# Kernel optimization log

Measured on AMD Instinct MI355X. Metric: run time of the kernel, lower is better.

The kernel has to match this reference:

```python
import jax, jax.numpy as jnp
import numpy as np

N, T, D, K = 32, 8192, 64, 64
LOG2PI = float(np.log(2.0 * np.pi))


def setup_inputs() -> dict:
    key = jax.random.key(0)
    k1, k2, k3, k4 = jax.random.split(key, 4)
    x = jax.random.normal(k1, (N, T, D), dtype=jnp.float32)
    # valid GMM params: positive weights summing to 1, positive diagonal covariances
    weights = jax.nn.softmax(jax.random.normal(k2, (K,), dtype=jnp.float32))
    means = jax.random.normal(k3, (K, D), dtype=jnp.float32)
    covars = jax.random.uniform(k4, (K, D), dtype=jnp.float32, minval=0.5, maxval=1.5)
    return {"x": x, "weights": weights, "means": means, "covars": covars}


def _posterior(x, weights, means, covars):
    # diagonal-GMM predict_proba without materializing [N,T,K,D]:
    # sum_d (x-mu)^2/c = sum x^2/c - 2 sum x*mu/c + sum mu^2/c
    inv_c = 1.0 / covars                                   # [K,D]
    quad = (jnp.einsum('ntd,kd->ntk', x * x, inv_c)
            - 2.0 * jnp.einsum('ntd,kd->ntk', x, means * inv_c)
            + jnp.sum(means * means * inv_c, axis=-1))      # [N,T,K]
    log_prob = (jnp.log(weights)
                - 0.5 * (D * LOG2PI + jnp.sum(jnp.log(covars), axis=-1) + quad))
    return jax.nn.softmax(log_prob, axis=-1)               # [N,T,K]


def reference(x, weights, means, covars):
    # p = predict_proba * weights, renormalized over K (as in the torch code)
    p = _posterior(x, weights, means, covars) * weights
    p = p / jnp.sum(p, axis=-1, keepdims=True)             # [N,T,K]

    # pooled statistics over T (einsum avoids the [N,T,K,D] intermediate)
    s0 = jnp.sum(p, axis=1)                                # [N,K]
    s1 = jnp.einsum('ntk,ntd->nkd', p, x)                  # [N,K,D]
    s2 = jnp.einsum('ntk,ntd->nkd', p, x * x)              # [N,K,D]

    sw = jnp.sqrt(weights)                                 # [K]
    v0 = (s0 - T * weights) / sw                           # [N,K]
    v1 = (s1 - means * s0[..., None]) / (sw[:, None] * jnp.sqrt(covars))
    v2 = (s2 - 2.0 * means * s1 + (means ** 2 - covars) * s0[..., None]) / (
        jnp.sqrt(jnp.float32(2.0)) * sw[:, None] * covars)

    v = jnp.concatenate([v0[..., None], v1, v2], axis=2).reshape(x.shape[0], -1)
    # power normalization then L2 normalization
    v = jnp.sign(v) * jnp.sqrt(jnp.abs(v))
    v = v / jnp.linalg.norm(v, axis=1, keepdims=True)
    return v
```

## Files before the change

kernel.cpp:

```cpp
#include <hip/hip_runtime.h>
#include <math.h>

#define N_  32
#define T_  8192
#define D_  64
#define K_  64
#define CHUNKS 24
#define TB 64
#define STATS_PER_N (K_ + 2 * K_ * D_)
#define XSTR 72

typedef _Float16 half_t;
typedef __attribute__((ext_vector_type(8)))  _Float16 v8h;
typedef __attribute__((ext_vector_type(4)))  float    v4f;
typedef __attribute__((ext_vector_type(16))) float    v16f;

__global__ void prep_kernel(const float* __restrict__ w, const float* __restrict__ mu,
                            const float* __restrict__ cv, float* __restrict__ Ap,
                            half_t* __restrict__ WH, float* __restrict__ ssq) {
    if (blockIdx.x < 8) {
#pragma unroll
        for (int i = 0; i < 4; ++i) {
            const int e = blockIdx.x * 1024 + i * 256 + threadIdx.x;
            const int j = e & 7, l = (e >> 3) & 63, fs = e >> 9;
            const int tile = fs >> 2, s = fs & 3;
            const int kc = 16 * tile + (l & 15);
            const int f  = 32 * s + 8 * (l >> 4) + j;
            float val;
            if (f < 64) val = mu[kc * 64 + f] / cv[kc * 64 + f];
            else        val = -0.5f / cv[kc * 64 + (f - 64)];
            WH[e] = (half_t)val;
        }
    } else {
        if (threadIdx.x < 32) ssq[threadIdx.x] = 0.f;
        if (threadIdx.x < K_) {
            const int k = threadIdx.x;
            float acc = 0.f;
            for (int d = 0; d < D_; ++d) {
                const int idx = k * D_ + d;
                const float c = cv[idx], m = mu[idx];
                acc += logf(c) + m * m / c;
            }
            Ap[k] = 2.f * logf(w[k]) - 0.5f * acc;
        }
    }
}

__launch_bounds__(256, 3)
__global__ void main_kernel(const float* __restrict__ x, const float* __restrict__ Ap,
                            const half_t* __restrict__ WH, float* __restrict__ outbuf,
                            int mode) {
    __shared__ half_t Xs[2][TB][XSTR];
    __shared__ half_t Pt[2][K_][XSTR];
    __shared__ float  s0sh[4][64];

    const int tid  = threadIdx.x;
    const int lane = tid & 63;
    const int wv   = tid >> 6;
    const int chunk = blockIdx.x;
    const int n     = blockIdx.y;
    const int q     = lane >> 4;
    const int c0    = lane & 15;
    const int tok   = 16 * wv + c0;

    const int r3   = (3 - (n % 3)) % 3;
    const int hcnt = (chunk + 2 - r3) / 3;
    const int boff = 5 * chunk + hcnt;
    const int cnt  = 5 + ((chunk % 3) == r3 ? 1 : 0);

    v8h Wf[16];
#pragma unroll
    for (int t = 0; t < 4; ++t)
#pragma unroll
        for (int s = 0; s < 4; ++s)
            Wf[t * 4 + s] = *(const v8h*)(WH + (size_t)((t * 4 + s) * 64 + lane) * 8);

    float apv[16];
#pragma unroll
    for (int t = 0; t < 4; ++t)
#pragma unroll
        for (int r = 0; r < 4; ++r) apv[t * 4 + r] = Ap[16 * t + 4 * q + r];

    float S0loc[16];
#pragma unroll
    for (int j = 0; j < 16; ++j) S0loc[j] = 0.f;

    const int sig = wv >> 1;
    const int dh  = wv & 1;
    v16f accB[2];
#pragma unroll
    for (int m = 0; m < 2; ++m)
#pragma unroll
        for (int r = 0; r < 16; ++r) accB[m][r] = 0.f;

    const size_t xbase = ((size_t)n * T_ + (size_t)boff * TB) * (size_t)D_;
    const float* xrow0 = x + xbase + tok * 64 + 8 * q;

    float4 R[4];
    R[0] = *(const float4*)(xrow0);
    R[1] = *(const float4*)(xrow0 + 4);
    R[2] = *(const float4*)(xrow0 + 32);
    R[3] = *(const float4*)(xrow0 + 36);

#pragma unroll 1
    for (int batch = 0; batch < cnt; ++batch) {
        const int buf = batch & 1;
        v8h xh0, xh1, qh0, qh1;
        {
            const float4 a = R[0], b = R[1], c = R[2], d = R[3];
            xh0[0] = (half_t)a.x; xh0[1] = (half_t)a.y; xh0[2] = (half_t)a.z; xh0[3] = (half_t)a.w;
            xh0[4] = (half_t)b.x; xh0[5] = (half_t)b.y; xh0[6] = (half_t)b.z; xh0[7] = (half_t)b.w;
            xh1[0] = (half_t)c.x; xh1[1] = (half_t)c.y; xh1[2] = (half_t)c.z; xh1[3] = (half_t)c.w;
            xh1[4] = (half_t)d.x; xh1[5] = (half_t)d.y; xh1[6] = (half_t)d.z; xh1[7] = (half_t)d.w;
            qh0[0] = (half_t)(a.x * a.x); qh0[1] = (half_t)(a.y * a.y);
            qh0[2] = (half_t)(a.z * a.z); qh0[3] = (half_t)(a.w * a.w);
            qh0[4] = (half_t)(b.x * b.x); qh0[5] = (half_t)(b.y * b.y);
            qh0[6] = (half_t)(b.z * b.z); qh0[7] = (half_t)(b.w * b.w);
            qh1[0] = (half_t)(c.x * c.x); qh1[1] = (half_t)(c.y * c.y);
            qh1[2] = (half_t)(c.z * c.z); qh1[3] = (half_t)(c.w * c.w);
            qh1[4] = (half_t)(d.x * d.x); qh1[5] = (half_t)(d.y * d.y);
            qh1[6] = (half_t)(d.z * d.z); qh1[7] = (half_t)(d.w * d.w);
            *(v8h*)&Xs[buf][tok][8 * q]      = xh0;
            *(v8h*)&Xs[buf][tok][32 + 8 * q] = xh1;
        }

        if (batch + 1 < cnt) {
            const float* xr = xrow0 + (size_t)(batch + 1) * TB * D_;
            R[0] = *(const float4*)(xr);
            R[1] = *(const float4*)(xr + 4);
            R[2] = *(const float4*)(xr + 32);
            R[3] = *(const float4*)(xr + 36);
        }

        {
            v4f acc[4];
#pragma unroll
            for (int t = 0; t < 4; ++t) acc[t] = (v4f)(0.f);
#pragma unroll
            for (int t = 0; t < 4; ++t) {
                acc[t] = __builtin_amdgcn_mfma_f32_16x16x32_f16(Wf[t * 4 + 0], xh0, acc[t], 0, 0, 0);
                acc[t] = __builtin_amdgcn_mfma_f32_16x16x32_f16(Wf[t * 4 + 1], xh1, acc[t], 0, 0, 0);
                acc[t] = __builtin_amdgcn_mfma_f32_16x16x32_f16(Wf[t * 4 + 2], qh0, acc[t], 0, 0, 0);
                acc[t] = __builtin_amdgcn_mfma_f32_16x16x32_f16(Wf[t * 4 + 3], qh1, acc[t], 0, 0, 0);
            }
            float pv[16];
            float m = -1e30f;
#pragma unroll
            for (int t = 0; t < 4; ++t)
#pragma unroll
                for (int r = 0; r < 4; ++r) {
                    const float lg = acc[t][r] + apv[t * 4 + r];
                    pv[t * 4 + r] = lg;
                    m = fmaxf(m, lg);
                }
            m = fmaxf(m, __shfl_xor(m, 16, 64));
            m = fmaxf(m, __shfl_xor(m, 32, 64));
            float ssum = 0.f;
#pragma unroll
            for (int j = 0; j < 16; ++j) { pv[j] = __expf(pv[j] - m); ssum += pv[j]; }
            ssum += __shfl_xor(ssum, 16, 64);
            ssum += __shfl_xor(ssum, 32, 64);
            const float rs = 1.f / ssum;
#pragma unroll
            for (int j = 0; j < 16; ++j) { pv[j] *= rs; S0loc[j] += pv[j]; }
#pragma unroll
            for (int t = 0; t < 4; ++t)
#pragma unroll
                for (int r = 0; r < 4; ++r)
                    Pt[buf][16 * t + 4 * q + r][tok] = (half_t)pv[t * 4 + r];
        }
        __syncthreads();

        {
            const int m   = lane & 31;
            const int h   = lane >> 5;
            const int d   = 32 * dh + m;
            const half_t* Arow0 = &Pt[buf][m][0];
            const half_t* Arow1 = &Pt[buf][32 + m][0];
            const half_t* Bsrc  = &Xs[buf][0][0];
#pragma unroll
            for (int st = 0; st < 4; ++st) {
                const int tB = 16 * st + 8 * h;
                const v8h a0 = *(const v8h*)(Arow0 + tB);
                const v8h a1 = *(const v8h*)(Arow1 + tB);
                v8h bf;
#pragma unroll
                for (int j = 0; j < 8; ++j)
                    bf[j] = Bsrc[(tB + j) * XSTR + d];
                if (sig) bf = bf * bf;
                accB[0] = __builtin_amdgcn_mfma_f32_32x32x16_f16(a0, bf, accB[0], 0, 0, 0);
                accB[1] = __builtin_amdgcn_mfma_f32_32x32x16_f16(a1, bf, accB[1], 0, 0, 0);
            }
        }
    }

    __syncthreads();
#pragma unroll
    for (int j = 0; j < 16; ++j) {
        float v = S0loc[j];
        v += __shfl_xor(v, 1, 64);
        v += __shfl_xor(v, 2, 64);
        v += __shfl_xor(v, 4, 64);
        v += __shfl_xor(v, 8, 64);
        S0loc[j] = v;
    }
    if (c0 == 0) {
#pragma unroll
        for (int t = 0; t < 4; ++t)
#pragma unroll
            for (int r = 0; r < 4; ++r)
                s0sh[wv][16 * t + 4 * q + r] = S0loc[t * 4 + r];
    }
    __syncthreads();

    if (mode == 1) {
        float* dstb = outbuf + (size_t)(n * CHUNKS + chunk) * STATS_PER_N;
        if (tid < 64)
            dstb[tid] = s0sh[0][tid] + s0sh[1][tid] + s0sh[2][tid] + s0sh[3][tid];
        const int d = 32 * dh + (lane & 31);
        float* dst = dstb + 64 + sig * 4096;
#pragma unroll
        for (int mt = 0; mt < 2; ++mt)
#pragma unroll
            for (int r = 0; r < 16; ++r) {
                const int kc = 32 * mt + (r & 3) + 8 * (r >> 2) + 4 * (lane >> 5);
                dst[kc * 64 + d] = accB[mt][r];
            }
    } else {
        float* sb = outbuf + (size_t)n * STATS_PER_N;
        if (tid < 64)
            atomicAdd(&sb[tid], s0sh[0][tid] + s0sh[1][tid] + s0sh[2][tid] + s0sh[3][tid]);
        const int d = 32 * dh + (lane & 31);
        float* dst = sb + 64 + sig * 4096;
#pragma unroll
        for (int mt = 0; mt < 2; ++mt)
#pragma unroll
            for (int r = 0; r < 16; ++r) {
                const int kc = 32 * mt + (r & 3) + 8 * (r >> 2) + 4 * (lane >> 5);
                atomicAdd(&dst[kc * 64 + d], accB[mt][r]);
            }
    }
}

__global__ void reduce_pow_kernel(const float* __restrict__ partials,
                                  const float* __restrict__ w, const float* __restrict__ mu,
                                  const float* __restrict__ cv,
                                  float* __restrict__ us, float* __restrict__ ssq) {
    __shared__ float red[4];
    const int e = blockIdx.x * 256 + threadIdx.x;
    const int n = blockIdx.y;
    float u = 0.f;
    if (e < STATS_PER_N) {
        const float* base = partials + (size_t)n * CHUNKS * STATS_PER_N;
        float sv = 0.f;
#pragma unroll 8
        for (int c = 0; c < CHUNKS; ++c) sv += base[(size_t)c * STATS_PER_N + e];
        float v; int oidx;
        if (e < 64) {
            const float wv = w[e];
            v = (sv - (float)T_ * wv) * rsqrtf(wv);
            oidx = e * 129;
        } else if (e < 64 + 4096) {
            const int idx = e - 64, k = idx >> 6, d = idx & 63;
            float s0v = 0.f;
#pragma unroll 8
            for (int c = 0; c < CHUNKS; ++c) s0v += base[(size_t)c * STATS_PER_N + k];
            v = (sv - mu[idx] * s0v) * rsqrtf(w[k] * cv[idx]);
            oidx = k * 129 + 1 + d;
        } else {
            const int idx = e - 4160, k = idx >> 6, d = idx & 63;
            float s0v = 0.f, s1v = 0.f;
#pragma unroll 4
            for (int c = 0; c < CHUNKS; ++c) {
                s0v += base[(size_t)c * STATS_PER_N + k];
                s1v += base[(size_t)c * STATS_PER_N + 64 + idx];
            }
            const float m_ = mu[idx], c_ = cv[idx];
            v = (sv - 2.f * m_ * s1v + (m_ * m_ - c_) * s0v) * (rsqrtf(2.f * w[k]) / c_);
            oidx = k * 129 + 65 + d;
        }
        u = (v >= 0.f) ? sqrtf(v) : -sqrtf(-v);
        us[(size_t)n * STATS_PER_N + oidx] = u;
    }
    float ss = u * u;
#pragma unroll
    for (int off = 32; off > 0; off >>= 1) ss += __shfl_xor(ss, off, 64);
    if ((threadIdx.x & 63) == 0) red[threadIdx.x >> 6] = ss;
    __syncthreads();
    if (threadIdx.x == 0)
        atomicAdd(&ssq[n], red[0] + red[1] + red[2] + red[3]);
}

__global__ void scale_kernel(const float* __restrict__ us, const float* __restrict__ ssq,
                             float* __restrict__ out) {
    const int e = blockIdx.x * 256 + threadIdx.x;
    const int n = blockIdx.y;
    if (e < STATS_PER_N)
        out[(size_t)n * STATS_PER_N + e] = us[(size_t)n * STATS_PER_N + e] * rsqrtf(ssq[n]);
}

__global__ void fin_kernel(const float* __restrict__ w, const float* __restrict__ mu,
                           const float* __restrict__ cv, const float* __restrict__ stats,
                           float* __restrict__ out) {
    __shared__ float us[STATS_PER_N];
    __shared__ float red[4];
    const int n   = blockIdx.x;
    const int tid = threadIdx.x;
    const float* sb = stats + (size_t)n * STATS_PER_N;

    float ss = 0.f;
    if (tid < 64) {
        const float wv = w[tid];
        const float v = (sb[tid] - (float)T_ * wv) * rsqrtf(wv);
        const float u = (v >= 0.f) ? sqrtf(v) : -sqrtf(-v);
        us[tid * 129] = u;
        ss = fmaf(u, u, ss);
    }
#pragma unroll 1
    for (int i = 0; i < 16; ++i) {
        const int idx = i * 256 + tid;
        const int k = idx >> 6, d = idx & 63;
        const float v = (sb[64 + idx] - mu[idx] * sb[k]) * rsqrtf(w[k] * cv[idx]);
        const float u = (v >= 0.f) ? sqrtf(v) : -sqrtf(-v);
        us[k * 129 + 1 + d] = u;
        ss = fmaf(u, u, ss);
    }
#pragma unroll 1
    for (int i = 0; i < 16; ++i) {
        const int idx = i * 256 + tid;
        const int k = idx >> 6, d = idx & 63;
        const float m_ = mu[idx], c_ = cv[idx];
        const float s1v = sb[64 + idx], s2v = sb[64 + 4096 + idx];
        const float v = (s2v - 2.f * m_ * s1v + (m_ * m_ - c_) * sb[k]) *
                        (rsqrtf(2.f * w[k]) / c_);
        const float u = (v >= 0.f) ? sqrtf(v) : -sqrtf(-v);
        us[k * 129 + 65 + d] = u;
        ss = fmaf(u, u, ss);
    }
#pragma unroll
    for (int off = 32; off > 0; off >>= 1) ss += __shfl_xor(ss, off, 64);
    if ((tid & 63) == 0) red[tid >> 6] = ss;
    __syncthreads();
    const float tot = red[0] + red[1] + red[2] + red[3];
    const float rn = rsqrtf(tot);
    for (int e = tid; e < STATS_PER_N; e += 256)
        out[(size_t)n * STATS_PER_N + e] = us[e] * rn;
}

extern "C" void kernel_launch(void* const* d_in, const int* in_sizes, int n_in,
                              void* d_out, int out_size, void* d_ws, size_t ws_size,
                              hipStream_t stream) {
    const float* x  = (const float*)d_in[0];
    const float* w  = (const float*)d_in[1];
    const float* mu = (const float*)d_in[2];
    const float* cv = (const float*)d_in[3];
    float* out = (float*)d_out;

    const size_t part_elems = (size_t)CHUNKS * N_ * STATS_PER_N;
    const size_t us_elems   = (size_t)N_ * STATS_PER_N;
    const size_t need_big = (part_elems + us_elems + 32 + K_ + (size_t)K_ * 64) * sizeof(float);

    if (ws_size >= need_big) {
        float* partials = (float*)d_ws;
        float* us  = partials + part_elems;
        float* ssq = us + us_elems;
        float* Ap  = ssq + 32;
        half_t* WH = (half_t*)(Ap + K_);

        prep_kernel<<<9, 256, 0, stream>>>(w, mu, cv, Ap, WH, ssq);
        main_kernel<<<dim3(CHUNKS, N_), 256, 0, stream>>>(x, Ap, WH, partials, 1);
        reduce_pow_kernel<<<dim3(33, N_), 256, 0, stream>>>(partials, w, mu, cv, us, ssq);
        scale_kernel<<<dim3(33, N_), 256, 0, stream>>>(us, ssq, out);
    } else {
        float* stats = (float*)d_ws;
        float* ssq = stats + us_elems;
        float* Ap  = ssq + 32;
        half_t* WH = (half_t*)(Ap + K_);

        hipMemsetAsync(stats, 0, us_elems * sizeof(float), stream);
        prep_kernel<<<9, 256, 0, stream>>>(w, mu, cv, Ap, WH, ssq);
        main_kernel<<<dim3(CHUNKS, N_), 256, 0, stream>>>(x, Ap, WH, stats, 0);
        fin_kernel<<<N_, 256, 0, stream>>>(w, mu, cv, stats, out);
    }
}
```

Measured before the change: 150.5 us.

## Split main kernel into producer and consumer waves with skewed pipeline

Waves 0-1 now act as producers. Each handles two 16-token groups: it converts x to fp16, runs the logit MFMAs and the softmax, and writes P and X to LDS. Waves 2-3 act as consumers and accumulate the s1 and s2 MFMAs for the previous batch. This lets both stages overlap with one barrier per step. It also folds the Ap bias into the accumulator init, squares x in half precision, and uses a lighter LDS-only barrier. The intended gain is overlapping the two phases, at the cost of less parallelism per stage, higher register pressure in consumers (four 32x32 accumulators), and an fp16 squaring precision change.

```diff
diff --git a/kernel.cpp b/kernel.cpp
--- a/kernel.cpp
+++ b/kernel.cpp
@@ -14,6 +14,11 @@
 typedef __attribute__((ext_vector_type(8)))  _Float16 v8h;
 typedef __attribute__((ext_vector_type(4)))  float    v4f;
 typedef __attribute__((ext_vector_type(16))) float    v16f;
+
+#define BAR_LDS() do {                                                  \
+    asm volatile("s_waitcnt lgkmcnt(0)" ::: "memory");                  \
+    __builtin_amdgcn_s_barrier();                                       \
+} while (0)
 
 __global__ void prep_kernel(const float* __restrict__ w, const float* __restrict__ mu,
                             const float* __restrict__ cv, float* __restrict__ Ap,
@@ -52,193 +57,204 @@
                             int mode) {
     __shared__ half_t Xs[2][TB][XSTR];
     __shared__ half_t Pt[2][K_][XSTR];
-    __shared__ float  s0sh[4][64];
+    __shared__ float  s0sh[2][64];
 
     const int tid  = threadIdx.x;
     const int lane = tid & 63;
     const int wv   = tid >> 6;
     const int chunk = blockIdx.x;
     const int n     = blockIdx.y;
-    const int q     = lane >> 4;
-    const int c0    = lane & 15;
-    const int tok   = 16 * wv + c0;
+    const int q    = lane >> 4;
+    const int c0   = lane & 15;
 
     const int r3   = (3 - (n % 3)) % 3;
     const int hcnt = (chunk + 2 - r3) / 3;
     const int boff = 5 * chunk + hcnt;
     const int cnt  = 5 + ((chunk % 3) == r3 ? 1 : 0);
 
-    v8h Wf[16];
-#pragma unroll
-    for (int t = 0; t < 4; ++t)
-#pragma unroll
-        for (int s = 0; s < 4; ++s)
-            Wf[t * 4 + s] = *(const v8h*)(WH + (size_t)((t * 4 + s) * 64 + lane) * 8);
-
-    float apv[16];
-#pragma unroll
-    for (int t = 0; t < 4; ++t)
-#pragma unroll
-        for (int r = 0; r < 4; ++r) apv[t * 4 + r] = Ap[16 * t + 4 * q + r];
-
+    const size_t xbase = ((size_t)n * T_ + (size_t)boff * TB) * (size_t)D_;
+    const bool producer = (wv < 2);
+    const int  sig = wv - 2;
+
+    v8h  Wf[16];
+    v4f  apv4[4];
     float S0loc[16];
-#pragma unroll
-    for (int j = 0; j < 16; ++j) S0loc[j] = 0.f;
-
-    const int sig = wv >> 1;
-    const int dh  = wv & 1;
-    v16f accB[2];
-#pragma unroll
-    for (int m = 0; m < 2; ++m)
-#pragma unroll
-        for (int r = 0; r < 16; ++r) accB[m][r] = 0.f;
-
-    const size_t xbase = ((size_t)n * T_ + (size_t)boff * TB) * (size_t)D_;
-    const float* xrow0 = x + xbase + tok * 64 + 8 * q;
-
-    float4 R[4];
-    R[0] = *(const float4*)(xrow0);
-    R[1] = *(const float4*)(xrow0 + 4);
-    R[2] = *(const float4*)(xrow0 + 32);
-    R[3] = *(const float4*)(xrow0 + 36);
+    float4 RA[4], RB[4];
+    const float* xrowA = nullptr;
+    const float* xrowB = nullptr;
+
+    v16f accB[2][2];
+
+    if (producer) {
+#pragma unroll
+        for (int t = 0; t < 4; ++t)
+#pragma unroll
+            for (int s = 0; s < 4; ++s)
+                Wf[t * 4 + s] = *(const v8h*)(WH + (size_t)((t * 4 + s) * 64 + lane) * 8);
+#pragma unroll
+        for (int t = 0; t < 4; ++t) apv4[t] = *(const v4f*)(Ap + 16 * t + 4 * q);
+#pragma unroll
+        for (int j = 0; j < 16; ++j) S0loc[j] = 0.f;
+        xrowA = x + xbase + (size_t)(16 * (2 * wv)     + c0) * 64 + 8 * q;
+        xrowB = x + xbase + (size_t)(16 * (2 * wv + 1) + c0) * 64 + 8 * q;
+        RA[0] = *(const float4*)(xrowA);      RA[1] = *(const float4*)(xrowA + 4);
+        RA[2] = *(const float4*)(xrowA + 32); RA[3] = *(const float4*)(xrowA + 36);
+        RB[0] = *(const float4*)(xrowB);      RB[1] = *(const float4*)(xrowB + 4);
+        RB[2] = *(const float4*)(xrowB + 32); RB[3] = *(const float4*)(xrowB + 36);
+    } else {
+#pragma unroll
+        for (int a = 0; a < 2; ++a)
+#pragma unroll
+            for (int bb = 0; bb < 2; ++bb)
+#pragma unroll
+                for (int r = 0; r < 16; ++r) accB[a][bb][r] = 0.f;
+    }
 
 #pragma unroll 1
-    for (int batch = 0; batch < cnt; ++batch) {
-        const int buf = batch & 1;
-        v8h xh0, xh1, qh0, qh1;
-        {
-            const float4 a = R[0], b = R[1], c = R[2], d = R[3];
-            xh0[0] = (half_t)a.x; xh0[1] = (half_t)a.y; xh0[2] = (half_t)a.z; xh0[3] = (half_t)a.w;
-            xh0[4] = (half_t)b.x; xh0[5] = (half_t)b.y; xh0[6] = (half_t)b.z; xh0[7] = (half_t)b.w;
-            xh1[0] = (half_t)c.x; xh1[1] = (half_t)c.y; xh1[2] = (half_t)c.z; xh1[3] = (half_t)c.w;
-            xh1[4] = (half_t)d.x; xh1[5] = (half_t)d.y; xh1[6] = (half_t)d.z; xh1[7] = (half_t)d.w;
-            qh0[0] = (half_t)(a.x * a.x); qh0[1] = (half_t)(a.y * a.y);
-            qh0[2] = (half_t)(a.z * a.z); qh0[3] = (half_t)(a.w * a.w);
-            qh0[4] = (half_t)(b.x * b.x); qh0[5] = (half_t)(b.y * b.y);
-            qh0[6] = (half_t)(b.z * b.z); qh0[7] = (half_t)(b.w * b.w);
-            qh1[0] = (half_t)(c.x * c.x); qh1[1] = (half_t)(c.y * c.y);
-            qh1[2] = (half_t)(c.z * c.z); qh1[3] = (half_t)(c.w * c.w);
-            qh1[4] = (half_t)(d.x * d.x); qh1[5] = (half_t)(d.y * d.y);
-            qh1[6] = (half_t)(d.z * d.z); qh1[7] = (half_t)(d.w * d.w);
-            *(v8h*)&Xs[buf][tok][8 * q]      = xh0;
-            *(v8h*)&Xs[buf][tok][32 + 8 * q] = xh1;
-        }
-
-        if (batch + 1 < cnt) {
-            const float* xr = xrow0 + (size_t)(batch + 1) * TB * D_;
-            R[0] = *(const float4*)(xr);
-            R[1] = *(const float4*)(xr + 4);
-            R[2] = *(const float4*)(xr + 32);
-            R[3] = *(const float4*)(xr + 36);
-        }
-
-        {
-            v4f acc[4];
-#pragma unroll
-            for (int t = 0; t < 4; ++t) acc[t] = (v4f)(0.f);
-#pragma unroll
-            for (int t = 0; t < 4; ++t) {
-                acc[t] = __builtin_amdgcn_mfma_f32_16x16x32_f16(Wf[t * 4 + 0], xh0, acc[t], 0, 0, 0);
-                acc[t] = __builtin_amdgcn_mfma_f32_16x16x32_f16(Wf[t * 4 + 1], xh1, acc[t], 0, 0, 0);
-                acc[t] = __builtin_amdgcn_mfma_f32_16x16x32_f16(Wf[t * 4 + 2], qh0, acc[t], 0, 0, 0);
-                acc[t] = __builtin_amdgcn_mfma_f32_16x16x32_f16(Wf[t * 4 + 3], qh1, acc[t], 0, 0, 0);
+    for (int b = 0; b <= cnt; ++b) {
+        if (producer && b < cnt) {
+            const int buf = b & 1;
+#pragma unroll
+            for (int g = 0; g < 2; ++g) {
+                float4* Rg = g ? RB : RA;
+                const int tok = 16 * (2 * wv + g) + c0;
+                v8h xh0, xh1, qh0, qh1;
+                {
+                    const float4 a = Rg[0], bq = Rg[1], c = Rg[2], d = Rg[3];
+                    xh0[0] = (half_t)a.x;  xh0[1] = (half_t)a.y;  xh0[2] = (half_t)a.z;  xh0[3] = (half_t)a.w;
+                    xh0[4] = (half_t)bq.x; xh0[5] = (half_t)bq.y; xh0[6] = (half_t)bq.z; xh0[7] = (half_t)bq.w;
+                    xh1[0] = (half_t)c.x;  xh1[1] = (half_t)c.y;  xh1[2] = (half_t)c.z;  xh1[3] = (half_t)c.w;
+                    xh1[4] = (half_t)d.x;  xh1[5] = (half_t)d.y;  xh1[6] = (half_t)d.z;  xh1[7] = (half_t)d.w;
+                    qh0 = xh0 * xh0;
+                    qh1 = xh1 * xh1;
+                    *(v8h*)&Xs[buf][tok][8 * q]      = xh0;
+                    *(v8h*)&Xs[buf][tok][32 + 8 * q] = xh1;
+                }
+                if (b + 1 < cnt) {
+                    const float* xr = (g ? xrowB : xrowA) + (size_t)(b + 1) * TB * D_;
+                    Rg[0] = *(const float4*)(xr);
+                    Rg[1] = *(const float4*)(xr + 4);
+                    Rg[2] = *(const float4*)(xr + 32);
+                    Rg[3] = *(const float4*)(xr + 36);
+                }
+                v4f acc[4];
+#pragma unroll
+                for (int t = 0; t < 4; ++t) acc[t] = apv4[t];
+#pragma unroll
+                for (int t = 0; t < 4; ++t) {
+                    acc[t] = __builtin_amdgcn_mfma_f32_16x16x32_f16(Wf[t * 4 + 0], xh0, acc[t], 0, 0, 0);
+                    acc[t] = __builtin_amdgcn_mfma_f32_16x16x32_f16(Wf[t * 4 + 1], xh1, acc[t], 0, 0, 0);
+                    acc[t] = __builtin_amdgcn_mfma_f32_16x16x32_f16(Wf[t * 4 + 2], qh0, acc[t], 0, 0, 0);
+                    acc[t] = __builtin_amdgcn_mfma_f32_16x16x32_f16(Wf[t * 4 + 3], qh1, acc[t], 0, 0, 0);
+                }
+                float pv[16];
+                float m = -1e30f;
+#pragma unroll
+                for (int t = 0; t < 4; ++t)
+#pragma unroll
+                    for (int r = 0; r < 4; ++r) {
+                        pv[t * 4 + r] = acc[t][r];
+                        m = fmaxf(m, acc[t][r]);
+                    }
+                m = fmaxf(m, __shfl_xor(m, 16, 64));
+                m = fmaxf(m, __shfl_xor(m, 32, 64));
+                float ssum = 0.f;
+#pragma unroll
+                for (int j = 0; j < 16; ++j) { pv[j] = __expf(pv[j] - m); ssum += pv[j]; }
+                ssum += __shfl_xor(ssum, 16, 64);
+                ssum += __shfl_xor(ssum, 32, 64);
+                const float rs = 1.f / ssum;
+#pragma unroll
+                for (int j = 0; j < 16; ++j) { pv[j] *= rs; S0loc[j] += pv[j]; }
+#pragma unroll
+                for (int t = 0; t < 4; ++t)
+#pragma unroll
+                    for (int r = 0; r < 4; ++r)
+                        Pt[buf][16 * t + 4 * q + r][tok] = (half_t)pv[t * 4 + r];
             }
-            float pv[16];
-            float m = -1e30f;
-#pragma unroll
-            for (int t = 0; t < 4; ++t)
-#pragma unroll
-                for (int r = 0; r < 4; ++r) {
-                    const float lg = acc[t][r] + apv[t * 4 + r];
-                    pv[t * 4 + r] = lg;
-                    m = fmaxf(m, lg);
-                }
-            m = fmaxf(m, __shfl_xor(m, 16, 64));
-            m = fmaxf(m, __shfl_xor(m, 32, 64));
-            float ssum = 0.f;
-#pragma unroll
-            for (int j = 0; j < 16; ++j) { pv[j] = __expf(pv[j] - m); ssum += pv[j]; }
-            ssum += __shfl_xor(ssum, 16, 64);
-            ssum += __shfl_xor(ssum, 32, 64);
-            const float rs = 1.f / ssum;
-#pragma unroll
-            for (int j = 0; j < 16; ++j) { pv[j] *= rs; S0loc[j] += pv[j]; }
-#pragma unroll
-            for (int t = 0; t < 4; ++t)
-#pragma unroll
-                for (int r = 0; r < 4; ++r)
-                    Pt[buf][16 * t + 4 * q + r][tok] = (half_t)pv[t * 4 + r];
-        }
-        __syncthreads();
-
-        {
-            const int m   = lane & 31;
-            const int h   = lane >> 5;
-            const int d   = 32 * dh + m;
+        }
+        if (!producer && b > 0) {
+            const int buf = (b - 1) & 1;
+            const int m = lane & 31;
+            const int h = lane >> 5;
             const half_t* Arow0 = &Pt[buf][m][0];
             const half_t* Arow1 = &Pt[buf][32 + m][0];
-            const half_t* Bsrc  = &Xs[buf][0][0];
+            const half_t* Bs    = &Xs[buf][0][0];
 #pragma unroll
             for (int st = 0; st < 4; ++st) {
-                const int tB = 16 * st + 8 * h;
-                const v8h a0 = *(const v8h*)(Arow0 + tB);
-                const v8h a1 = *(const v8h*)(Arow1 + tB);
-                v8h bf;
-#pragma unroll
-                for (int j = 0; j < 8; ++j)
-                    bf[j] = Bsrc[(tB + j) * XSTR + d];
-                if (sig) bf = bf * bf;
-                accB[0] = __builtin_amdgcn_mfma_f32_32x32x16_f16(a0, bf, accB[0], 0, 0, 0);
-                accB[1] = __builtin_amdgcn_mfma_f32_32x32x16_f16(a1, bf, accB[1], 0, 0, 0);
+                const int tBk = 16 * st + 8 * h;
+                const v8h a0 = *(const v8h*)(Arow0 + tBk);
+                const v8h a1 = *(const v8h*)(Arow1 + tBk);
+#pragma unroll
+                for (int dhf = 0; dhf < 2; ++dhf) {
+                    const int d = 32 * dhf + m;
+                    v8h bf;
+#pragma unroll
+                    for (int j = 0; j < 8; ++j)
+                        bf[j] = Bs[(tBk + j) * XSTR + d];
+                    if (sig) bf = bf * bf;
+                    accB[0][dhf] = __builtin_amdgcn_mfma_f32_32x32x16_f16(a0, bf, accB[0][dhf], 0, 0, 0);
+                    accB[1][dhf] = __builtin_amdgcn_mfma_f32_32x32x16_f16(a1, bf, accB[1][dhf], 0, 0, 0);
+                }
             }
         }
-    }
-
-    __syncthreads();
-#pragma unroll
-    for (int j = 0; j < 16; ++j) {
-        float v = S0loc[j];
-        v += __shfl_xor(v, 1, 64);
-        v += __shfl_xor(v, 2, 64);
-        v += __shfl_xor(v, 4, 64);
-        v += __shfl_xor(v, 8, 64);
-        S0loc[j] = v;
-    }
-    if (c0 == 0) {
-#pragma unroll
-        for (int t = 0; t < 4; ++t)
-#pragma unroll
-            for (int r = 0; r < 4; ++r)
-                s0sh[wv][16 * t + 4 * q + r] = S0loc[t * 4 + r];
+        BAR_LDS();
+    }
+
+    if (producer) {
+#pragma unroll
+        for (int j = 0; j < 16; ++j) {
+            float v = S0loc[j];
+            v += __shfl_xor(v, 1, 64);
+            v += __shfl_xor(v, 2, 64);
+            v += __shfl_xor(v, 4, 64);
+            v += __shfl_xor(v, 8, 64);
+            S0loc[j] = v;
+        }
+        if (c0 == 0) {
+#pragma unroll
+            for (int t = 0; t < 4; ++t)
+#pragma unroll
+                for (int r = 0; r < 4; ++r)
+                    s0sh[wv][16 * t + 4 * q + r] = S0loc[t * 4 + r];
+        }
     }
     __syncthreads();
 
     if (mode == 1) {
         float* dstb = outbuf + (size_t)(n * CHUNKS + chunk) * STATS_PER_N;
         if (tid < 64)
-            dstb[tid] = s0sh[0][tid] + s0sh[1][tid] + s0sh[2][tid] + s0sh[3][tid];
-        const int d = 32 * dh + (lane & 31);
-        float* dst = dstb + 64 + sig * 4096;
-#pragma unroll
-        for (int mt = 0; mt < 2; ++mt)
-#pragma unroll
-            for (int r = 0; r < 16; ++r) {
-                const int kc = 32 * mt + (r & 3) + 8 * (r >> 2) + 4 * (lane >> 5);
-                dst[kc * 64 + d] = accB[mt][r];
-            }
+            dstb[tid] = s0sh[0][tid] + s0sh[1][tid];
+        if (!producer) {
+            float* dst = dstb + 64 + sig * 4096;
+#pragma unroll
+            for (int mt = 0; mt < 2; ++mt)
+#pragma unroll
+                for (int dhf = 0; dhf < 2; ++dhf)
+#pragma unroll
+                    for (int r = 0; r < 16; ++r) {
+                        const int kc = 32 * mt + (r & 3) + 8 * (r >> 2) + 4 * (lane >> 5);
+                        const int d  = 32 * dhf + (lane & 31);
+                        dst[kc * 64 + d] = accB[mt][dhf][r];
+                    }
+        }
     } else {
         float* sb = outbuf + (size_t)n * STATS_PER_N;
         if (tid < 64)
-            atomicAdd(&sb[tid], s0sh[0][tid] + s0sh[1][tid] + s0sh[2][tid] + s0sh[3][tid]);
-        const int d = 32 * dh + (lane & 31);
-        float* dst = sb + 64 + sig * 4096;
-#pragma unroll
-        for (int mt = 0; mt < 2; ++mt)
-#pragma unroll
-            for (int r = 0; r < 16; ++r) {
-                const int kc = 32 * mt + (r & 3) + 8 * (r >> 2) + 4 * (lane >> 5);
-                atomicAdd(&dst[kc * 64 + d], accB[mt][r]);
-            }
+            atomicAdd(&sb[tid], s0sh[0][tid] + s0sh[1][tid]);
+        if (!producer) {
+            float* dst = sb + 64 + sig * 4096;
+#pragma unroll
+            for (int mt = 0; mt < 2; ++mt)
+#pragma unroll
+                for (int dhf = 0; dhf < 2; ++dhf)
+#pragma unroll
+                    for (int r = 0; r < 16; ++r) {
+                        const int kc = 32 * mt + (r & 3) + 8 * (r >> 2) + 4 * (lane >> 5);
+                        const int d  = 32 * dhf + (lane & 31);
+                        atomicAdd(&dst[kc * 64 + d], accB[mt][dhf][r]);
+                    }
+        }
     }
 }
 
```

New measurement: 204.3 us. 1.36x slower.
